# Kernel tuning notes

Hardware: AMD Instinct MI355X
Metric: run time of the kernel (lower is better)

Reference implementation:

```python
import jax, jax.numpy as jnp
import numpy as np

LN_EPS = 1e-5

def layer_norm(x, w, b):
    mu = jnp.mean(x, axis=-1, keepdims=True)
    var = jnp.mean(jnp.square(x - mu), axis=-1, keepdims=True)
    return (x - mu) * jax.lax.rsqrt(var + LN_EPS) * w + b

def adaptive_mask_np(aa, bb, ada_para=0.2):
    # True = disallowed (matches torch ~bool mask). Static shapes -> numpy.
    adaptive_num = int(bb * ada_para)
    cc = bb // aa
    i = np.arange(aa)
    start = i * cc
    end = start + cc + adaptive_num
    over = end > bb - 1
    start = np.where(over, np.maximum(start - (end - (bb - 1)), 0), start)
    end = np.where(over, bb, end)
    cols = np.arange(bb)
    allowed = (cols[None, :] >= start[:, None]) & (cols[None, :] < end[:, None])
    return jnp.asarray(~allowed)  # [aa, bb] bool

def setup_inputs() -> dict:
    key = jax.random.key(0)
    ks = jax.random.split(key, 20)
    Lq, Lk, B, d, dff = 512, 4096, 4, 512, 2048
    s = lambda k, shape: jax.random.normal(k, shape, dtype=jnp.float32) * 0.02
    inp = {
        'tgt': jax.random.normal(ks[0], (Lq, B, d), dtype=jnp.float32),
        'memory': jax.random.normal(ks[1], (Lk, B, d), dtype=jnp.float32),
        'Wq': s(ks[2], (d, d)), 'bq': jnp.zeros((d,), jnp.float32),
        'Wk': s(ks[3], (d, d)), 'bk': jnp.zeros((d,), jnp.float32),
        'Wv': s(ks[4], (d, d)), 'bv': jnp.zeros((d,), jnp.float32),
        'Wo': s(ks[5], (d, d)), 'bo': jnp.zeros((d,), jnp.float32),
        'W1': s(ks[6], (dff, d)), 'b1': jnp.zeros((dff,), jnp.float32),
        'W2': s(ks[7], (d, dff)), 'b2': jnp.zeros((d,), jnp.float32),
        'ln1_w': jnp.ones((d,), jnp.float32), 'ln1_b': jnp.zeros((d,), jnp.float32),
        'ln2_w': jnp.ones((d,), jnp.float32), 'ln2_b': jnp.zeros((d,), jnp.float32),
        'ln3_w': jnp.ones((d,), jnp.float32), 'ln3_b': jnp.zeros((d,), jnp.float32),
        'ln4_w': jnp.ones((d,), jnp.float32), 'ln4_b': jnp.zeros((d,), jnp.float32),
    }
    return inp

def reference(tgt, memory, Wq, bq, Wk, bk, Wv, bv, Wo, bo, W1, b1, W2, b2,
              ln1_w, ln1_b, ln2_w, ln2_b, ln3_w, ln3_b, ln4_w, ln4_b):
    Lq, B, d = tgt.shape
    Lk = memory.shape[0]
    H = 8
    hd = d // H
    scale = 1.0 / jnp.sqrt(jnp.asarray(hd, tgt.dtype))

    t = layer_norm(tgt, ln1_w, ln1_b)      # [Lq,B,d]
    m = layer_norm(memory, ln2_w, ln2_b)   # [Lk,B,d]

    mask = adaptive_mask_np(Lq, Lk, 0.2)   # [Lq,Lk] bool, True=masked

    q = (t @ Wq.T + bq).reshape(Lq, B, H, hd)
    k = (m @ Wk.T + bk).reshape(Lk, B, H, hd)
    v = (m @ Wv.T + bv).reshape(Lk, B, H, hd)

    scores = jnp.einsum('qbhd,kbhd->bhqk', q * scale, k)
    scores = jnp.where(mask[None, None], -jnp.inf, scores)
    p = jax.nn.softmax(scores, axis=-1)                   # [B,H,Lq,Lk]
    attn_weights = jnp.mean(p, axis=1)                    # [B,Lq,Lk] (avg over heads)

    ctx = jnp.einsum('bhqk,kbhd->qbhd', p, v).reshape(Lq, B, d)
    tgt2 = ctx @ Wo.T + bo

    x = t + tgt2                       # dropout1 = identity (eval)
    x = layer_norm(x, ln3_w, ln3_b)
    ff = jax.nn.relu(x @ W1.T + b1) @ W2.T + b2
    x = x + ff                         # dropout2 = identity (eval)
    x = layer_norm(x, ln4_w, ln4_b)
    return (x, attn_weights)
```

## Files before the change

kernel.cpp:

```cpp
#include <hip/hip_runtime.h>
#include <hip/hip_bf16.h>

typedef __hip_bfloat16 bf16_t;
typedef __bf16 bf16x8 __attribute__((ext_vector_type(8)));
typedef float f32x4 __attribute__((ext_vector_type(4)));

#define LQ 512
#define LK 4096
#define BATCH 4
#define DMODEL 512
#define NHEAD 8
#define HEADDIM 64
#define DFF 2048
#define LN_EPS 1e-5f

#define KSTR 2080
#define VSTR 4128

__device__ inline float tofl(float x) { return x; }
__device__ inline float tofl(bf16_t x) { return __bfloat162float(x); }
__device__ inline void stfl(float* p, float v) { *p = v; }
__device__ inline void stfl(bf16_t* p, float v) { *p = __float2bfloat16(v); }

__device__ __forceinline__ void gld_lds16(const bf16_t* g, void* lds_base) {
    __builtin_amdgcn_global_load_lds(
        (const __attribute__((address_space(1))) uint32_t*)g,
        (__attribute__((address_space(3))) uint32_t*)lds_base, 16, 0, 0);
}

template <typename TOUT, bool DUAL>
__global__ void ln_kernel(const float* __restrict__ in, const float* __restrict__ w,
                          const float* __restrict__ b, TOUT* __restrict__ out1,
                          float* __restrict__ out2) {
    __shared__ float red[256];
    const int row = blockIdx.x;
    const int tid = threadIdx.x;
    const float* x = in + (size_t)row * DMODEL;
    float v0 = x[tid];
    float v1 = x[tid + 256];

    red[tid] = v0 + v1;
    __syncthreads();
    for (int s = 128; s > 0; s >>= 1) { if (tid < s) red[tid] += red[tid + s]; __syncthreads(); }
    float mu = red[0] * (1.0f / DMODEL);
    __syncthreads();

    float d0 = v0 - mu, d1 = v1 - mu;
    red[tid] = d0 * d0 + d1 * d1;
    __syncthreads();
    for (int s = 128; s > 0; s >>= 1) { if (tid < s) red[tid] += red[tid + s]; __syncthreads(); }
    float inv = rsqrtf(red[0] * (1.0f / DMODEL) + LN_EPS);

    float r0 = d0 * inv * w[tid] + b[tid];
    float r1 = d1 * inv * w[tid + 256] + b[tid + 256];
    TOUT* o = out1 + (size_t)row * DMODEL;
    stfl(&o[tid], r0);
    stfl(&o[tid + 256], r1);
    if (DUAL) {
        float* o2 = out2 + (size_t)row * DMODEL;
        o2[tid] = r0;
        o2[tid + 256] = r1;
    }
}

__global__ void ln12_prep_kernel(const float* __restrict__ tgt, const float* __restrict__ memory,
                                 const float* __restrict__ w1, const float* __restrict__ b1,
                                 const float* __restrict__ w2, const float* __restrict__ b2,
                                 bf16_t* __restrict__ t_bf, float* __restrict__ t_f32,
                                 bf16_t* __restrict__ m_buf,
                                 const float* __restrict__ s0, const float* __restrict__ s1,
                                 const float* __restrict__ s2, const float* __restrict__ s3,
                                 const float* __restrict__ s4,
                                 bf16_t* __restrict__ wqkvo, bf16_t* __restrict__ w1bf) {
    const int row = blockIdx.x;
    const int tid = threadIdx.x;
    if (row >= 18432) {
        int t = (row - 18432) * 256 + tid;
        int which = t >> 16;
        int idx = (t & 65535) * 4;
        const float* s; bf16_t* d;
        if (which < 4) {
            s = (which == 0 ? s0 : which == 1 ? s1 : which == 2 ? s2 : s3);
            d = wqkvo + (size_t)which * 262144;
        } else {
            s = s4 + (size_t)(which - 4) * 262144;
            d = w1bf + (size_t)(which - 4) * 262144;
        }
        float4 v = *(const float4*)(s + idx);
        d[idx + 0] = __float2bfloat16(v.x);
        d[idx + 1] = __float2bfloat16(v.y);
        d[idx + 2] = __float2bfloat16(v.z);
        d[idx + 3] = __float2bfloat16(v.w);
        return;
    }
    __shared__ float red[256];
    const float* in; const float* w; const float* b;
    bf16_t* o1; float* o2; bool dual;
    if (row < 2048) {
        in = tgt + (size_t)row * DMODEL; w = w1; b = b1;
        o1 = t_bf + (size_t)row * DMODEL; o2 = t_f32 + (size_t)row * DMODEL; dual = true;
    } else {
        int r2 = row - 2048;
        in = memory + (size_t)r2 * DMODEL; w = w2; b = b2;
        o1 = m_buf + (size_t)r2 * DMODEL; o2 = nullptr; dual = false;
    }
    float v0 = in[tid];
    float v1 = in[tid + 256];
    red[tid] = v0 + v1;
    __syncthreads();
    for (int s = 128; s > 0; s >>= 1) { if (tid < s) red[tid] += red[tid + s]; __syncthreads(); }
    float mu = red[0] * (1.0f / DMODEL);
    __syncthreads();
    float d0 = v0 - mu, d1 = v1 - mu;
    red[tid] = d0 * d0 + d1 * d1;
    __syncthreads();
    for (int s = 128; s > 0; s >>= 1) { if (tid < s) red[tid] += red[tid + s]; __syncthreads(); }
    float inv = rsqrtf(red[0] * (1.0f / DMODEL) + LN_EPS);
    float r0 = d0 * inv * w[tid] + b[tid];
    float r1 = d1 * inv * w[tid + 256] + b[tid + 256];
    o1[tid] = __float2bfloat16(r0);
    o1[tid + 256] = __float2bfloat16(r1);
    if (dual) {
        o2[tid] = r0;
        o2[tid + 256] = r1;
    }
}

template <typename TC, bool RELU, bool RESID>
__global__ __launch_bounds__(256) void gemm64(
        const bf16_t* __restrict__ A, const bf16_t* __restrict__ B,
        const float* __restrict__ bias, const float* __restrict__ resid,
        TC* __restrict__ C, int M, int N, int K) {
    __shared__ uint4 As4[512];
    __shared__ uint4 Bs4[512];

    const int tid = threadIdx.x;
    const int lane = tid & 63;
    const int wave = tid >> 6;
    const int row16 = lane & 15;
    const int quad = lane >> 4;
    const int n0 = blockIdx.x * 64;
    const int m0 = blockIdx.y * 64;

    const int wy = wave >> 1;
    const int wx = wave & 1;
    const int m_base = wy * 32;
    const int n_base = wx * 32;

    const int rr = lane >> 3;
    const int kc = (lane & 7) ^ rr;
    const int kx = row16 & 7;

    const bf16_t* AsE = (const bf16_t*)As4;
    const bf16_t* BsE = (const bf16_t*)Bs4;

    f32x4 acc[2][2] = {};

    for (int k0 = 0; k0 < K; k0 += 64) {
#pragma unroll
        for (int it = 0; it < 2; it++) {
            int issue = it * 4 + wave;
            int r = issue * 8 + rr;
            gld_lds16(A + (size_t)(m0 + r) * K + k0 + kc * 8, &As4[issue * 64]);
        }
#pragma unroll
        for (int it = 0; it < 2; it++) {
            int issue = it * 4 + wave;
            int r = issue * 8 + rr;
            gld_lds16(B + (size_t)(n0 + r) * K + k0 + kc * 8, &Bs4[issue * 64]);
        }
        __syncthreads();
#pragma unroll
        for (int s = 0; s < 2; s++) {
            const int kq = s * 4 + quad;
            const int kcs = (kq ^ kx) * 8;
            bf16x8 af[2], bfr[2];
#pragma unroll
            for (int i = 0; i < 2; i++)
                af[i] = *(const bf16x8*)&AsE[(m_base + i * 16 + row16) * 64 + kcs];
#pragma unroll
            for (int j = 0; j < 2; j++)
                bfr[j] = *(const bf16x8*)&BsE[(n_base + j * 16 + row16) * 64 + kcs];
#pragma unroll
            for (int i = 0; i < 2; i++)
#pragma unroll
                for (int j = 0; j < 2; j++)
                    acc[i][j] = __builtin_amdgcn_mfma_f32_16x16x32_bf16(af[i], bfr[j], acc[i][j], 0, 0, 0);
        }
        __syncthreads();
    }

#pragma unroll
    for (int i = 0; i < 2; i++) {
#pragma unroll
        for (int j = 0; j < 2; j++) {
            int col = n0 + n_base + j * 16 + row16;
            float bsv = bias[col];
#pragma unroll
            for (int r = 0; r < 4; r++) {
                int row = m0 + m_base + i * 16 + quad * 4 + r;
                float val = acc[i][j][r] + bsv;
                if (RESID) val += resid[(size_t)row * N + col];
                if (RELU) val = fmaxf(val, 0.0f);
                stfl(&C[(size_t)row * N + col], val);
            }
        }
    }
}

__global__ __launch_bounds__(256) void proj_qkv(
        const bf16_t* __restrict__ At, const bf16_t* __restrict__ Am,
        const bf16_t* __restrict__ BQ, const bf16_t* __restrict__ BK,
        const bf16_t* __restrict__ BV, const float* __restrict__ biasq,
        const float* __restrict__ biask, const float* __restrict__ biasv,
        bf16_t* __restrict__ CQ, bf16_t* __restrict__ CK, bf16_t* __restrict__ CV) {
    __shared__ uint4 As4[1024];
    __shared__ uint4 Bs4[1024];

    const int bid = blockIdx.x;
    const int tid = threadIdx.x;
    const int lane = tid & 63;
    const int wave = tid >> 6;
    const int row16 = lane & 15;
    const int quad = lane >> 4;
    const int rr = lane >> 3;
    const int kc = (lane & 7) ^ rr;
    const int kx = row16 & 7;

    const bf16_t* AsE = (const bf16_t*)As4;
    const bf16_t* BsE = (const bf16_t*)Bs4;

    if (bid < 1024) {
        const bool isV = (bid >> 9) != 0;
        const int within = bid & 511;
        const int n0 = (within & 3) * 128;
        const int m0 = (within >> 2) * 128;
        const bf16_t* B = isV ? BV : BK;
        const float* bias = isV ? biasv : biask;

        const int wy = wave >> 1;
        const int wx = wave & 1;
        const int m_base = wy * 64;
        const int n_base = wx * 64;

        f32x4 acc[4][4] = {};

        for (int k0 = 0; k0 < DMODEL; k0 += 64) {
#pragma unroll
            for (int it = 0; it < 4; it++) {
                int issue = it * 4 + wave;
                int r = issue * 8 + rr;
                gld_lds16(Am + (size_t)(m0 + r) * DMODEL + k0 + kc * 8, &As4[issue * 64]);
            }
#pragma unroll
            for (int it = 0; it < 4; it++) {
                int issue = it * 4 + wave;
                int r = issue * 8 + rr;
                gld_lds16(B + (size_t)(n0 + r) * DMODEL + k0 + kc * 8, &Bs4[issue * 64]);
            }
            __syncthreads();
#pragma unroll
            for (int s = 0; s < 2; s++) {
                const int kq = s * 4 + quad;
                const int kcs = (kq ^ kx) * 8;
                bf16x8 af[4], bfr[4];
#pragma unroll
                for (int i = 0; i < 4; i++)
                    af[i] = *(const bf16x8*)&AsE[(m_base + i * 16 + row16) * 64 + kcs];
#pragma unroll
                for (int j = 0; j < 4; j++)
                    bfr[j] = *(const bf16x8*)&BsE[(n_base + j * 16 + row16) * 64 + kcs];
#pragma unroll
                for (int i = 0; i < 4; i++)
#pragma unroll
                    for (int j = 0; j < 4; j++)
                        acc[i][j] = __builtin_amdgcn_mfma_f32_16x16x32_bf16(af[i], bfr[j], acc[i][j], 0, 0, 0);
            }
            __syncthreads();
        }

#pragma unroll
        for (int i = 0; i < 4; i++) {
#pragma unroll
            for (int j = 0; j < 4; j++) {
                int col = n0 + n_base + j * 16 + row16;
                float bsv = bias[col];
#pragma unroll
                for (int r = 0; r < 4; r++) {
                    int row = m0 + m_base + i * 16 + quad * 4 + r;
                    float val = acc[i][j][r] + bsv;
                    if (isV) {
                        CV[(size_t)row * DMODEL + col] = __float2bfloat16(val);
                    } else {
                        CK[(size_t)(row >> 2) * KSTR + (size_t)(row & 3) * 512 + col] =
                            __float2bfloat16(val);
                    }
                }
            }
        }
    } else {
        const int q = bid - 1024;
        const int n0 = (q & 7) * 64;
        const int m0 = (q >> 3) * 64;

        const int wy = wave >> 1;
        const int wx = wave & 1;
        const int m_base = wy * 32;
        const int n_base = wx * 32;

        f32x4 acc[2][2] = {};

        for (int k0 = 0; k0 < DMODEL; k0 += 64) {
#pragma unroll
            for (int it = 0; it < 2; it++) {
                int issue = it * 4 + wave;
                int r = issue * 8 + rr;
                gld_lds16(At + (size_t)(m0 + r) * DMODEL + k0 + kc * 8, &As4[issue * 64]);
            }
#pragma unroll
            for (int it = 0; it < 2; it++) {
                int issue = it * 4 + wave;
                int r = issue * 8 + rr;
                gld_lds16(BQ + (size_t)(n0 + r) * DMODEL + k0 + kc * 8, &Bs4[issue * 64]);
            }
            __syncthreads();
#pragma unroll
            for (int s = 0; s < 2; s++) {
                const int kq = s * 4 + quad;
                const int kcs = (kq ^ kx) * 8;
                bf16x8 af[2], bfr[2];
#pragma unroll
                for (int i = 0; i < 2; i++)
                    af[i] = *(const bf16x8*)&AsE[(m_base + i * 16 + row16) * 64 + kcs];
#pragma unroll
                for (int j = 0; j < 2; j++)
                    bfr[j] = *(const bf16x8*)&BsE[(n_base + j * 16 + row16) * 64 + kcs];
#pragma unroll
                for (int i = 0; i < 2; i++)
#pragma unroll
                    for (int j = 0; j < 2; j++)
                        acc[i][j] = __builtin_amdgcn_mfma_f32_16x16x32_bf16(af[i], bfr[j], acc[i][j], 0, 0, 0);
            }
            __syncthreads();
        }

#pragma unroll
        for (int i = 0; i < 2; i++) {
#pragma unroll
            for (int j = 0; j < 2; j++) {
                int col = n0 + n_base + j * 16 + row16;
                float bsv = biasq[col];
#pragma unroll
                for (int r = 0; r < 4; r++) {
                    int row = m0 + m_base + i * 16 + quad * 4 + r;
                    CQ[(size_t)row * DMODEL + col] = __float2bfloat16(acc[i][j][r] + bsv);
                }
            }
        }
    }
}

__global__ __launch_bounds__(256) void post_kv(const bf16_t* __restrict__ kb,
                                               bf16_t* __restrict__ kT,
                                               const float* __restrict__ w2s,
                                               bf16_t* __restrict__ w2d) {
    __shared__ bf16_t tile[64][80];
    const int bid = blockIdx.x;
    const int t = threadIdx.x;
    if (bid >= 2048) {
        int i = ((bid - 2048) * 256 + t) * 4;
        float4 v = *(const float4*)(w2s + i);
        w2d[i + 0] = __float2bfloat16(v.x);
        w2d[i + 1] = __float2bfloat16(v.y);
        w2d[i + 2] = __float2bfloat16(v.z);
        w2d[i + 3] = __float2bfloat16(v.w);
        return;
    }
    const int kt = (bid & 63) * 64;
    const int ct = ((bid >> 6) & 7) * 64;
    const int b  = bid >> 9;
    {
        int kl = t >> 2, cl = (t & 3) * 16;
        const bf16_t* src = kb + ((size_t)(kt + kl) * 4 + b) * 512 + ct + cl;
        *(uint4*)&tile[kl][cl]     = *(const uint4*)src;
        *(uint4*)&tile[kl][cl + 8] = *(const uint4*)(src + 8);
    }
    __syncthreads();
    {
        int cl2 = t >> 2, ks = (t & 3) * 16;
        __attribute__((aligned(16))) bf16_t vals[16];
#pragma unroll
        for (int j = 0; j < 16; j++) vals[j] = tile[ks + j][cl2];
        bf16_t* dst = kT + ((size_t)b * 512 + ct + cl2) * VSTR + kt + ks;
        *(uint4*)dst       = *(const uint4*)&vals[0];
        *(uint4*)(dst + 8) = *(const uint4*)&vals[8];
    }
}

__device__ __forceinline__ void qk_issue(const bf16_t* kb_base, int us, int g,
                                         int row16, bf16x8 (&b0)[8], bf16x8 (&b1)[8]) {
#pragma unroll
    for (int j = 0; j < 8; ++j) {
        int key = us + (g * 8 + j) * 16 + row16;
        int key_eff = key > 4095 ? 4095 : key;
        const bf16_t* kr = kb_base + (size_t)key_eff * KSTR;
        b0[j] = *(const bf16x8*)kr;
        b1[j] = *(const bf16x8*)(kr + 32);
    }
}

__device__ __forceinline__ void qk_compute(int g, bf16x8 (&b0)[8], bf16x8 (&b1)[8],
        const bf16x8 aq0, const bf16x8 aq1, float (&l)[4], bf16_t* PsH,
        int row16, int quad, const int (&sq)[4], const int (&eq)[4], int us) {
    __builtin_amdgcn_s_setprio(1);
#pragma unroll
    for (int j = 0; j < 8; ++j) {
        int it = g * 8 + j;
        f32x4 acc = {};
        acc = __builtin_amdgcn_mfma_f32_16x16x32_bf16(aq0, b0[j], acc, 0, 0, 0);
        acc = __builtin_amdgcn_mfma_f32_16x16x32_bf16(aq1, b1[j], acc, 0, 0, 0);
        int key = us + it * 16 + row16;
#pragma unroll
        for (int r = 0; r < 4; r++) {
            int ql = quad * 4 + r;
            bool valid = (key >= sq[r]) && (key < eq[r]);
            float p = valid ? __expf(0.125f * acc[r]) : 0.0f;
            l[r] += p;
            if (ql < 8) PsH[ql * 904 + it * 16 + row16] = __float2bfloat16(p);
        }
    }
    __builtin_amdgcn_s_setprio(0);
}

__device__ __forceinline__ void pv_issue(const bf16_t* vbase, int g, int row16, int quad,
                                         bf16x8 (&vb)[4][4]) {
#pragma unroll
    for (int j = 0; j < 4; ++j) {
        int it = g * 4 + j;
#pragma unroll
        for (int nt = 0; nt < 4; ++nt)
            vb[j][nt] = *(const bf16x8*)(vbase + (size_t)(nt * 16 + row16) * VSTR
                                         + it * 32 + quad * 8);
    }
}

__device__ __forceinline__ void pv_compute(int g, bf16x8 (&vb)[4][4], const bf16_t* PsH,
        const bf16_t* Zrow, int row16, int quad, f32x4 (&o)[4]) {
    __builtin_amdgcn_s_setprio(1);
#pragma unroll
    for (int j = 0; j < 4; ++j) {
        int it = g * 4 + j;
        const bf16_t* ap_src = (row16 < 8) ? &PsH[row16 * 904 + it * 32 + quad * 8]
                                           : &Zrow[0];
        bf16x8 ap = *(const bf16x8*)ap_src;
#pragma unroll
        for (int nt = 0; nt < 4; ++nt)
            o[nt] = __builtin_amdgcn_mfma_f32_16x16x32_bf16(ap, vb[j][nt], o[nt], 0, 0, 0);
    }
    __builtin_amdgcn_s_setprio(0);
}

__global__ __launch_bounds__(512, 1) void attn_mfma(
        const bf16_t* __restrict__ qb,
        const bf16_t* __restrict__ kb,
        const bf16_t* __restrict__ vT,
        bf16_t* __restrict__ ctx,
        float* __restrict__ attn_out) {
    extern __shared__ char smem[];
    bf16_t* Ps   = (bf16_t*)smem;
    bf16_t* Qs   = (bf16_t*)(smem + 115712);
    bf16_t* Zrow = (bf16_t*)(smem + 115712 + 8320);
    float*  Ls   = (float*)(smem + 115712 + 8320 + 1808);

    const int blk = blockIdx.x;
    const int b  = (blk & 7) >> 1;
    const int qt = ((blk >> 3) << 1) | (blk & 1);
    const int q0 = qt * 8;
    const int tid = threadIdx.x;
    const int lane = tid & 63;
    const int h = tid >> 6;
    const int hoffg = h * HEADDIM;
    const int row16 = lane & 15;
    const int quad = lane >> 4;

    int us; { int s = q0 * 8, e = s + 827; if (e > 4095) s = 3268; us = s; }
    int sq[4], eq[4];
#pragma unroll
    for (int r = 0; r < 4; r++) {
        int ql = quad * 4 + r;
        if (ql < 8) {
            int s = (q0 + ql) * 8, e = s + 827;
            if (e > 4095) { s = 3268; e = 4096; }
            sq[r] = s; eq[r] = e;
        } else { sq[r] = 0; eq[r] = 0; }
    }

    {
        int r = tid >> 6, coff = (tid & 63) * 8;
        *(uint4*)&Qs[r * 520 + coff] =
            *(const uint4*)(qb + ((size_t)(q0 + r) * 4 + b) * 512 + coff);
        if (tid < 113) { uint4 z = {0, 0, 0, 0}; *(uint4*)&Zrow[tid * 8] = z; }
    }
    __syncthreads();

    const bf16_t* q0p = (row16 < 8) ? &Qs[row16 * 520 + hoffg + quad * 8] : &Zrow[0];
    const bf16_t* q1p = (row16 < 8) ? &Qs[row16 * 520 + hoffg + 32 + quad * 8] : &Zrow[8];
    const bf16x8 aq0 = *(const bf16x8*)q0p;
    const bf16x8 aq1 = *(const bf16x8*)q1p;

    bf16_t* PsH = Ps + h * 8 * 904;
    const bf16_t* kb_base = kb + b * 512 + hoffg + quad * 8;

    bf16x8 ka0[8], ka1[8], kc0[8], kc1[8];
    float l[4] = {0.f, 0.f, 0.f, 0.f};
    qk_issue(kb_base, us, 0, row16, ka0, ka1);
    for (int gg = 0; gg < 3; ++gg) {
        qk_issue(kb_base, us, 2 * gg + 1, row16, kc0, kc1);
        qk_compute(2 * gg, ka0, ka1, aq0, aq1, l, PsH, row16, quad, sq, eq, us);
        qk_issue(kb_base, us, 2 * gg + 2, row16, ka0, ka1);
        qk_compute(2 * gg + 1, kc0, kc1, aq0, aq1, l, PsH, row16, quad, sq, eq, us);
    }
    bf16x8 va[4][4], vb_[4][4];
    const bf16_t* vbase = vT + (size_t)(b * 512 + hoffg) * VSTR + us;
    pv_issue(vbase, 0, row16, quad, va);
    qk_compute(6, ka0, ka1, aq0, aq1, l, PsH, row16, quad, sq, eq, us);

#pragma unroll
    for (int off = 1; off < 16; off <<= 1) {
#pragma unroll
        for (int r = 0; r < 4; r++) l[r] += __shfl_xor(l[r], off, 64);
    }
    float linv[4];
#pragma unroll
    for (int r = 0; r < 4; r++) linv[r] = 1.0f / l[r];
    if (row16 == 0) {
#pragma unroll
        for (int r = 0; r < 4; r++) {
            int ql = quad * 4 + r;
            if (ql < 8) Ls[h * 8 + ql] = linv[r];
        }
    }

    f32x4 o[4] = {};
    for (int gg = 0; gg < 3; ++gg) {
        pv_issue(vbase, 2 * gg + 1, row16, quad, vb_);
        pv_compute(2 * gg, va, PsH, Zrow, row16, quad, o);
        pv_issue(vbase, 2 * gg + 2, row16, quad, va);
        pv_compute(2 * gg + 1, vb_, PsH, Zrow, row16, quad, o);
    }
    pv_compute(6, va, PsH, Zrow, row16, quad, o);

    __syncthreads();

    {
        int qq = h;
        float ls[8];
#pragma unroll
        for (int hh = 0; hh < 8; ++hh) ls[hh] = 0.125f * Ls[hh * 8 + qq];
        float* rowp = attn_out + ((size_t)b * LQ + q0 + qq) * LK;
        const bf16_t* ps = Ps + qq * 904;
        for (int it = 0; it < 16; ++it) {
            int c4 = (it * 64 + lane) * 4;
            float4 v = {0.f, 0.f, 0.f, 0.f};
            int off = c4 - us;
            if (off >= -3 && off < 896) {
#pragma unroll
                for (int e = 0; e < 4; ++e) {
                    int pc = off + e;
                    float s = 0.f;
                    if (pc >= 0 && pc < 896) {
#pragma unroll
                        for (int hh = 0; hh < 8; ++hh)
                            s += ls[hh] * tofl(ps[hh * 8 * 904 + pc]);
                    }
                    (&v.x)[e] = s;
                }
            }
            *(float4*)(rowp + c4) = v;
        }
    }

#pragma unroll
    for (int nt = 0; nt < 4; nt++) {
#pragma unroll
        for (int r = 0; r < 4; r++) {
            int ql = quad * 4 + r;
            if (ql < 8) {
                ctx[((size_t)(q0 + ql) * 4 + b) * 512 + hoffg + nt * 16 + row16] =
                    __float2bfloat16(o[nt][r] * linv[r]);
            }
        }
    }
}

extern "C" void kernel_launch(void* const* d_in, const int* in_sizes, int n_in,
                              void* d_out, int out_size, void* d_ws, size_t ws_size,
                              hipStream_t stream) {
    const float* tgt    = (const float*)d_in[0];
    const float* memory = (const float*)d_in[1];
    const float* Wq = (const float*)d_in[2];
    const float* bq = (const float*)d_in[3];
    const float* Wk = (const float*)d_in[4];
    const float* bk = (const float*)d_in[5];
    const float* Wv = (const float*)d_in[6];
    const float* bv = (const float*)d_in[7];
    const float* Wo = (const float*)d_in[8];
    const float* bo = (const float*)d_in[9];
    const float* W1 = (const float*)d_in[10];
    const float* b1 = (const float*)d_in[11];
    const float* W2 = (const float*)d_in[12];
    const float* b2 = (const float*)d_in[13];
    const float* ln1w = (const float*)d_in[14];
    const float* ln1b = (const float*)d_in[15];
    const float* ln2w = (const float*)d_in[16];
    const float* ln2b = (const float*)d_in[17];
    const float* ln3w = (const float*)d_in[18];
    const float* ln3b = (const float*)d_in[19];
    const float* ln4w = (const float*)d_in[20];
    const float* ln4b = (const float*)d_in[21];

    const size_t M1 = (size_t)LQ * BATCH;
    const size_t M2 = (size_t)LK * BATCH;
    const size_t SZ1 = M1 * DMODEL;

    char* wsb = (char*)d_ws;
    const size_t MB = 1 << 20;
    bf16_t* m_buf   = (bf16_t*)(wsb + 0 * MB);
    bf16_t* vT_buf  = (bf16_t*)(wsb + 0 * MB);
    bf16_t* h_buf   = (bf16_t*)(wsb + 0 * MB);
    bf16_t* k_buf   = (bf16_t*)(wsb + 17 * MB);
    float*  xres    = (float*)(wsb + 17 * MB);
    float*  xln_f   = (float*)(wsb + 21 * MB);
    float*  x2_buf  = (float*)(wsb + 25 * MB);
    bf16_t* xln_bf  = (bf16_t*)(wsb + 29 * MB);
    bf16_t* v_buf   = (bf16_t*)(wsb + 34 * MB);
    bf16_t* t_bf    = (bf16_t*)(wsb + 50 * MB);
    bf16_t* W2_bf   = (bf16_t*)(wsb + 50 * MB);
    float*  t_f32   = (float*)(wsb + 52 * MB);
    bf16_t* q_bf    = (bf16_t*)(wsb + 56 * MB);
    bf16_t* ctx_buf = (bf16_t*)(wsb + 58 * MB);
    bf16_t* wqkvo   = (bf16_t*)(wsb + 60 * MB);
    bf16_t* W1_bf   = (bf16_t*)(wsb + 62 * MB);

    bf16_t* Wq_bf = wqkvo;
    bf16_t* Wk_bf = wqkvo + 262144;
    bf16_t* Wv_bf = wqkvo + 2 * 262144;
    bf16_t* Wo_bf = wqkvo + 3 * 262144;

    float* out_x    = (float*)d_out;
    float* out_attn = out_x + SZ1;

    ln12_prep_kernel<<<dim3(M1 + M2 + 2048), dim3(256), 0, stream>>>(
        tgt, memory, ln1w, ln1b, ln2w, ln2b, t_bf, t_f32, m_buf,
        Wq, Wk, Wv, Wo, W1, wqkvo, W1_bf);

    proj_qkv<<<dim3(1280), dim3(256), 0, stream>>>(
        t_bf, m_buf, Wq_bf, Wk_bf, Wv_bf, bq, bk, bv, q_bf, k_buf, v_buf);

    post_kv<<<dim3(3072), dim3(256), 0, stream>>>(v_buf, vT_buf, W2, W2_bf);

    const int attn_lds = 115712 + 8320 + 1808 + 256;
    hipFuncSetAttribute((const void*)attn_mfma,
                        hipFuncAttributeMaxDynamicSharedMemorySize, attn_lds);
    attn_mfma<<<dim3(256), dim3(512), attn_lds, stream>>>(
        q_bf, k_buf, vT_buf, ctx_buf, out_attn);

    gemm64<float, false, true><<<dim3(8, 32), dim3(256), 0, stream>>>(
        ctx_buf, Wo_bf, bo, t_f32, xres, M1, DMODEL, DMODEL);

    ln_kernel<bf16_t, true><<<dim3(M1), dim3(256), 0, stream>>>(xres, ln3w, ln3b, xln_bf, xln_f);

    gemm64<bf16_t, true, false><<<dim3(32, 32), dim3(256), 0, stream>>>(
        xln_bf, W1_bf, b1, nullptr, h_buf, M1, DFF, DMODEL);

    gemm64<float, false, true><<<dim3(8, 32), dim3(256), 0, stream>>>(
        h_buf, W2_bf, b2, xln_f, x2_buf, M1, DMODEL, DFF);

    ln_kernel<float, false><<<dim3(M1), dim3(256), 0, stream>>>(x2_buf, ln4w, ln4b, out_x, nullptr);
}
```

Before: 281.3 us.

## Fuse output projection, residual add and LayerNorm3 into attention kernel

The attention kernel no longer writes ctx to global memory. It keeps the 8-row context tile in LDS, multiplies it by Wo with MFMA, adds the bias and the t residual, and runs LayerNorm3 in place, writing xln in both bf16 and fp32. This removes two kernel launches and the ctx/xres round trips through global memory. In exchange, each of the 256 blocks reads the full Wo matrix from global/L2 with only 8 useful rows out of 16 in each MFMA tile, and the attention kernel's tail gets longer.

```diff
diff --git a/kernel.cpp b/kernel.cpp
--- a/kernel.cpp
+++ b/kernel.cpp
@@ -464,8 +464,13 @@
         const bf16_t* __restrict__ qb,
         const bf16_t* __restrict__ kb,
         const bf16_t* __restrict__ vT,
-        bf16_t* __restrict__ ctx,
-        float* __restrict__ attn_out) {
+        float* __restrict__ attn_out,
+        const bf16_t* __restrict__ WoB,
+        const float* __restrict__ bo,
+        const float* __restrict__ t_f32,
+        const float* __restrict__ ln3w, const float* __restrict__ ln3b,
+        bf16_t* __restrict__ xlnb,
+        float* __restrict__ xlnf) {
     extern __shared__ char smem[];
     bf16_t* Ps   = (bf16_t*)smem;
     bf16_t* Qs   = (bf16_t*)(smem + 115712);
@@ -552,6 +557,18 @@
 
     __syncthreads();
 
+    bf16_t* cs = Qs;
+#pragma unroll
+    for (int nt = 0; nt < 4; nt++) {
+#pragma unroll
+        for (int r = 0; r < 4; r++) {
+            int ql = quad * 4 + r;
+            if (ql < 8)
+                cs[ql * 520 + hoffg + nt * 16 + row16] =
+                    __float2bfloat16(o[nt][r] * linv[r]);
+        }
+    }
+
     {
         int qq = h;
         float ls[8];
@@ -579,16 +596,58 @@
             *(float4*)(rowp + c4) = v;
         }
     }
-
-#pragma unroll
-    for (int nt = 0; nt < 4; nt++) {
-#pragma unroll
-        for (int r = 0; r < 4; r++) {
-            int ql = quad * 4 + r;
-            if (ql < 8) {
-                ctx[((size_t)(q0 + ql) * 4 + b) * 512 + hoffg + nt * 16 + row16] =
-                    __float2bfloat16(o[nt][r] * linv[r]);
-            }
+    __syncthreads();
+
+    float* xrf = (float*)Ps;
+    {
+        f32x4 acc2[4] = {};
+        for (int k0 = 0; k0 < DMODEL; k0 += 32) {
+            const bf16_t* ap = (row16 < 8) ? &cs[row16 * 520 + k0 + quad * 8] : &Zrow[0];
+            bf16x8 af = *(const bf16x8*)ap;
+#pragma unroll
+            for (int j = 0; j < 4; j++) {
+                int col = h * 64 + j * 16 + row16;
+                bf16x8 bw = *(const bf16x8*)&WoB[(size_t)col * 512 + k0 + quad * 8];
+                acc2[j] = __builtin_amdgcn_mfma_f32_16x16x32_bf16(af, bw, acc2[j], 0, 0, 0);
+            }
+        }
+#pragma unroll
+        for (int j = 0; j < 4; j++) {
+#pragma unroll
+            for (int r = 0; r < 4; r++) {
+                int ql = quad * 4 + r;
+                if (ql < 8) {
+                    int col = h * 64 + j * 16 + row16;
+                    int rowg = (q0 + ql) * 4 + b;
+                    float val = acc2[j][r] + bo[col] + t_f32[(size_t)rowg * 512 + col];
+                    xrf[ql * 520 + col] = val;
+                }
+            }
+        }
+    }
+    __syncthreads();
+
+    {
+        int ql = h;
+        int rowg = (q0 + ql) * 4 + b;
+        float v[8]; float sum = 0.f;
+#pragma unroll
+        for (int e = 0; e < 8; e++) { v[e] = xrf[ql * 520 + e * 64 + lane]; sum += v[e]; }
+#pragma unroll
+        for (int off = 1; off < 64; off <<= 1) sum += __shfl_xor(sum, off, 64);
+        float mu = sum * (1.0f / DMODEL);
+        float sqs = 0.f;
+#pragma unroll
+        for (int e = 0; e < 8; e++) { float d = v[e] - mu; sqs += d * d; }
+#pragma unroll
+        for (int off = 1; off < 64; off <<= 1) sqs += __shfl_xor(sqs, off, 64);
+        float inv = rsqrtf(sqs * (1.0f / DMODEL) + LN_EPS);
+#pragma unroll
+        for (int e = 0; e < 8; e++) {
+            int col = e * 64 + lane;
+            float rres = (v[e] - mu) * inv * ln3w[col] + ln3b[col];
+            xlnb[(size_t)rowg * 512 + col] = __float2bfloat16(rres);
+            xlnf[(size_t)rowg * 512 + col] = rres;
         }
     }
 }
@@ -620,7 +679,6 @@
     const float* ln4b = (const float*)d_in[21];
 
     const size_t M1 = (size_t)LQ * BATCH;
-    const size_t M2 = (size_t)LK * BATCH;
     const size_t SZ1 = M1 * DMODEL;
 
     char* wsb = (char*)d_ws;
@@ -629,18 +687,20 @@
     bf16_t* vT_buf  = (bf16_t*)(wsb + 0 * MB);
     bf16_t* h_buf   = (bf16_t*)(wsb + 0 * MB);
     bf16_t* k_buf   = (bf16_t*)(wsb + 17 * MB);
-    float*  xres    = (float*)(wsb + 17 * MB);
-    float*  xln_f   = (float*)(wsb + 21 * MB);
     float*  x2_buf  = (float*)(wsb + 25 * MB);
-    bf16_t* xln_bf  = (bf16_t*)(wsb + 29 * MB);
-    bf16_t* v_buf   = (bf16_t*)(wsb + 34 * MB);
+    float*  xln_f   = (float*)(wsb + 34 * MB);
+    bf16_t* v_buf   = (bf16_t*)(wsb + 38 * MB);
     bf16_t* t_bf    = (bf16_t*)(wsb + 50 * MB);
     bf16_t* W2_bf   = (bf16_t*)(wsb + 50 * MB);
     float*  t_f32   = (float*)(wsb + 52 * MB);
     bf16_t* q_bf    = (bf16_t*)(wsb + 56 * MB);
-    bf16_t* ctx_buf = (bf16_t*)(wsb + 58 * MB);
+    bf16_t* xln_bf  = (bf16_t*)(wsb + 58 * MB);
     bf16_t* wqkvo   = (bf16_t*)(wsb + 60 * MB);
     bf16_t* W1_bf   = (bf16_t*)(wsb + 62 * MB);
+
+    v_buf  = (bf16_t*)(wsb + 34 * MB);
+    xln_f  = (float*)(wsb + 34 * MB);
+    x2_buf = (float*)(wsb + 25 * MB);
 
     bf16_t* Wq_bf = wqkvo;
     bf16_t* Wk_bf = wqkvo + 262144;
@@ -650,7 +710,7 @@
     float* out_x    = (float*)d_out;
     float* out_attn = out_x + SZ1;
 
-    ln12_prep_kernel<<<dim3(M1 + M2 + 2048), dim3(256), 0, stream>>>(
+    ln12_prep_kernel<<<dim3(M1 + 16384 + 2048), dim3(256), 0, stream>>>(
         tgt, memory, ln1w, ln1b, ln2w, ln2b, t_bf, t_f32, m_buf,
         Wq, Wk, Wv, Wo, W1, wqkvo, W1_bf);
 
@@ -663,12 +723,8 @@
     hipFuncSetAttribute((const void*)attn_mfma,
                         hipFuncAttributeMaxDynamicSharedMemorySize, attn_lds);
     attn_mfma<<<dim3(256), dim3(512), attn_lds, stream>>>(
-        q_bf, k_buf, vT_buf, ctx_buf, out_attn);
-
-    gemm64<float, false, true><<<dim3(8, 32), dim3(256), 0, stream>>>(
-        ctx_buf, Wo_bf, bo, t_f32, xres, M1, DMODEL, DMODEL);
-
-    ln_kernel<bf16_t, true><<<dim3(M1), dim3(256), 0, stream>>>(xres, ln3w, ln3b, xln_bf, xln_f);
+        q_bf, k_buf, vT_buf, out_attn, Wo_bf, bo, t_f32, ln3w, ln3b,
+        xln_bf, xln_f);
 
     gemm64<bf16_t, true, false><<<dim3(32, 32), dim3(256), 0, stream>>>(
         xln_bf, W1_bf, b1, nullptr, h_buf, M1, DFF, DMODEL);
```

After: 286.7 us. No clear change (+1.9%).
